# Kernel tuning notes

Measured on AMD Instinct MI355X. Metric: run time of the kernel, lower is better.

## Reference

```python
import jax, jax.numpy as jnp
import numpy as np

B, S, D, H = 8, 1024, 768, 12
DH = D // H  # 64
PATCHES = S  # module's `patches` arg; rows >= patches//2 are zeroed pre-softmax


def setup_inputs() -> dict:
    key = jax.random.key(0)
    ks = jax.random.split(key, 5)
    sc = 1.0 / np.sqrt(D)
    return {
        "hidden_states": jax.random.normal(ks[0], (B, S, D), dtype=jnp.float32),
        "Wq": jax.random.normal(ks[1], (D, D), dtype=jnp.float32) * sc,
        "bq": jnp.zeros((D,), dtype=jnp.float32),
        "Wk": jax.random.normal(ks[2], (D, D), dtype=jnp.float32) * sc,
        "bk": jnp.zeros((D,), dtype=jnp.float32),
        "Wv": jax.random.normal(ks[3], (D, D), dtype=jnp.float32) * sc,
        "bv": jnp.zeros((D,), dtype=jnp.float32),
        "Wo": jax.random.normal(ks[4], (D, D), dtype=jnp.float32) * sc,
        "bo": jnp.zeros((D,), dtype=jnp.float32),
    }


def _split_heads(x):
    # [B,S,D] -> [B,H,S,DH]
    b, s, _ = x.shape
    return x.reshape(b, s, H, DH).transpose(0, 2, 1, 3)


def reference(hidden_states, Wq, bq, Wk, bk, Wv, bv, Wo, bo):
    # self-attention path (kv=None), mask=None path, eval-mode dropout (identity)
    q = _split_heads(hidden_states @ Wq + bq)
    k = _split_heads(hidden_states @ Wk + bk)
    v = _split_heads(hidden_states @ Wv + bv)
    scores = jnp.einsum("bhqd,bhkd->bhqk", q, k) / np.sqrt(DH)
    # custom masking: zero out all score rows for query positions >= patches//2
    scores = scores.at[:, :, PATCHES // 2 :, :].set(0.0)
    probs = jax.nn.softmax(scores, axis=-1)
    ctx = jnp.einsum("bhqk,bhkd->bhqd", probs, v)
    ctx = ctx.transpose(0, 2, 1, 3).reshape(hidden_states.shape[0], -1, D)
    return ctx @ Wo + bo  # vis=False -> weights not returned
```

## Files before the change

kernel.cpp:

```cpp
#include <hip/hip_runtime.h>
#include <hip/hip_bf16.h>
#include <cstdint>


typedef __bf16 bf16_t;
typedef bf16_t bf16x8 __attribute__((ext_vector_type(8)));
typedef float f32x4 __attribute__((ext_vector_type(4)));

#define QSCALE 0.18033688011112042f

__device__ __forceinline__ f32x4 mfma16(bf16x8 a, bf16x8 b, f32x4 c) {
  return __builtin_amdgcn_mfma_f32_16x16x32_bf16(a, b, c, 0, 0, 0);
}
__device__ __forceinline__ unsigned packbf(float x, float y) {
  union { bf16_t h; unsigned short u; } a, b;
  a.h = (bf16_t)x; b.h = (bf16_t)y;
  return (unsigned)a.u | ((unsigned)b.u << 16);
}
__device__ __forceinline__ unsigned short tobf(float x) {
  union { bf16_t h; unsigned short u; } a; a.h = (bf16_t)x; return a.u;
}
__device__ __forceinline__ void glds16(const void* g, void* s) {
  __builtin_amdgcn_global_load_lds((const __attribute__((address_space(1))) void*)g,
                                   (__attribute__((address_space(3))) void*)s, 16, 0, 0);
}

__global__ __launch_bounds__(256) void k_cvt_x(const float* __restrict__ X,
                                               unsigned short* __restrict__ Xbf) {
  int i = blockIdx.x * 256 + threadIdx.x;
  const float4* p = (const float4*)X;
  float4 a = p[2 * i], b = p[2 * i + 1];
  uint4 o;
  o.x = packbf(a.x, a.y); o.y = packbf(a.z, a.w);
  o.z = packbf(b.x, b.y); o.w = packbf(b.z, b.w);
  ((uint4*)Xbf)[i] = o;
}

__global__ __launch_bounds__(256) void k_wtrans(const float* __restrict__ Wq,
                                                const float* __restrict__ Wk,
                                                const float* __restrict__ Wv,
                                                const float* __restrict__ Wo,
                                                unsigned short* __restrict__ Wt) {
  int which = blockIdx.z;
  const float* W = (which == 0) ? Wq : (which == 1) ? Wk : (which == 2) ? Wv : Wo;
  __shared__ float tile[64][65];
  int k0 = blockIdx.x * 64, n0 = blockIdx.y * 64;
  int t = threadIdx.x;
  int c = t & 63, r0 = t >> 6;
#pragma unroll
  for (int i = 0; i < 16; ++i) {
    int r = r0 + i * 4;
    tile[r][c] = W[(size_t)(k0 + r) * 768 + n0 + c];
  }
  __syncthreads();
#pragma unroll
  for (int i = 0; i < 16; ++i) {
    int nr = r0 + i * 4;
    Wt[(size_t)(which * 768 + n0 + nr) * 768 + k0 + c] = tobf(tile[c][nr]);
  }
}

__global__ __launch_bounds__(256) void k_gemm_qkv(
    const unsigned short* __restrict__ Xbf, const unsigned short* __restrict__ Wt,
    const float* __restrict__ bq, const float* __restrict__ bk, const float* __restrict__ bv,
    unsigned short* __restrict__ Qw, unsigned short* __restrict__ Kw,
    unsigned short* __restrict__ Vt) {
  __shared__ __align__(16) unsigned short As[4096], Bs[4096];
  int id = blockIdx.x;
  int mt, nt;
  if (id < 576) { int mf = id / 18; mt = ((mf >> 2) << 3) + (mf & 3); nt = id - mf * 18; }
  else { int j = id - 576; int mh = j / 12; mt = ((mh >> 2) << 3) + 4 + (mh & 3); nt = 6 + (j - mh * 12); }
  const int m0 = mt * 128, n0 = nt * 128;
  const int tid = threadIdx.x, w = tid >> 6, l = tid & 63, lr = l & 15, lg = l >> 4;
  const int wm = w >> 1, wn = w & 1;
  const unsigned short* gA = Xbf + (size_t)(m0 + (tid >> 2)) * 768 + (tid & 3) * 8;
  const unsigned short* gB = Wt + (size_t)(n0 + (tid >> 2)) * 768 + (tid & 3) * 8;
  unsigned short* sA = As + w * 512;
  unsigned short* sB = Bs + w * 512;
  const unsigned short* rA = As + (wm * 64 + lr) * 32 + lg * 8;
  const unsigned short* rB = Bs + (wn * 64 + lr) * 32 + lg * 8;
  f32x4 acc[4][4] = {};
  for (int kt = 0; kt < 24; ++kt) {
    const int ko = kt * 32;
    glds16(gA + ko, sA);            glds16(gA + 64 * 768 + ko, sA + 2048);
    glds16(gB + ko, sB);            glds16(gB + 64 * 768 + ko, sB + 2048);
    __syncthreads();
    bf16x8 af[4], bfr[4];
#pragma unroll
    for (int i = 0; i < 4; ++i) af[i] = *(const bf16x8*)(rA + i * 512);
#pragma unroll
    for (int i = 0; i < 4; ++i) bfr[i] = *(const bf16x8*)(rB + i * 512);
#pragma unroll
    for (int i = 0; i < 4; ++i)
#pragma unroll
      for (int j = 0; j < 4; ++j) acc[i][j] = mfma16(af[i], bfr[j], acc[i][j]);
    __syncthreads();
  }
  const int rbase = m0 + wm * 64 + lg * 4;
  const int cbase = n0 + wn * 64 + lr;
#pragma unroll
  for (int nf = 0; nf < 4; ++nf) {
    const int n = cbase + nf * 16;
#pragma unroll
    for (int mf = 0; mf < 4; ++mf) {
      const int r = rbase + mf * 16;
      const int b = r >> 10, s = r & 1023;
      if (n < 768) {
        const int h = n >> 6, dh = n & 63;
        const float bias = bq[n];
        unsigned short* qp = Qw + ((size_t)(b * 12 + h) * 512 + s) * 64 + dh;
#pragma unroll
        for (int rg = 0; rg < 4; ++rg)
          qp[(size_t)rg * 64] = tobf((acc[mf][nf][rg] + bias) * QSCALE);
      } else if (n < 1536) {
        const int d = n - 768, h = d >> 6, dh = d & 63;
        const float bias = bk[d];
        unsigned short* kp = Kw + ((size_t)(b * 12 + h) * 1024 + s) * 64 + dh;
#pragma unroll
        for (int rg = 0; rg < 4; ++rg)
          kp[(size_t)rg * 64] = tobf(acc[mf][nf][rg] + bias);
      } else {
        const int d = n - 1536, h = d >> 6, dh = d & 63;
        const float bias = bv[d];
        uint2 pv;
        pv.x = packbf(acc[mf][nf][0] + bias, acc[mf][nf][1] + bias);
        pv.y = packbf(acc[mf][nf][2] + bias, acc[mf][nf][3] + bias);
        *(uint2*)(Vt + ((size_t)(b * 12 + h) * 64 + dh) * 1024 + s) = pv;
      }
    }
  }
}

__global__ __launch_bounds__(256) void k_attn(const unsigned short* __restrict__ Qw,
                                              const unsigned short* __restrict__ Kw,
                                              const unsigned short* __restrict__ Vt,
                                              unsigned short* __restrict__ Ctx) {
  const int id = blockIdx.x;
  const int bh = id % 96;
  const int q0 = (id / 96) * 64;
  const int tid = threadIdx.x, w = tid >> 6, l = tid & 63, lr = l & 15, lg = l >> 4;
  const unsigned short* Qp = Qw + (size_t)bh * 512 * 64;
  const unsigned short* Kp = Kw + (size_t)bh * 1024 * 64;
  const unsigned short* Vp = Vt + (size_t)bh * 64 * 1024;

  __shared__ __align__(16) unsigned short Ks[2][4096];
  __shared__ __align__(16) unsigned short Vs[2][4096];
  __shared__ __align__(16) unsigned short P[4 * 16 * 72];

  const int j1 = 2 * w, j2 = 2 * w + 1;
  const int rA = j1 * 8 + (l >> 3), cA = (l & 7) ^ (rA & 7);
  const int rB = j2 * 8 + (l >> 3), cB = (l & 7) ^ (rB & 7);
  const unsigned short* kSrcA = Kp + rA * 64 + cA * 8;
  const unsigned short* kSrcB = Kp + rB * 64 + cB * 8;
  const unsigned short* vSrcA = Vp + rA * 1024 + cA * 8;
  const unsigned short* vSrcB = Vp + rB * 1024 + cB * 8;

  const int s0 = lr * 64 + ((lg ^ (lr & 7)) * 8);
  const int s1 = lr * 64 + (((lg + 4) ^ (lr & 7)) * 8);

  unsigned short* prow = P + (w * 16 + lr) * 72;
  const unsigned short* prd = prow + lg * 8;
  const int qrow = q0 + w * 16 + lr;
  const bf16x8 qf0 = *(const bf16x8*)(Qp + (size_t)qrow * 64 + lg * 8);
  const bf16x8 qf1 = *(const bf16x8*)(Qp + (size_t)qrow * 64 + 32 + lg * 8);

  f32x4 accc[4] = {};
  float z = 0.f;

  glds16(kSrcA, &Ks[0][j1 * 512]);
  glds16(kSrcB, &Ks[0][j2 * 512]);
  glds16(vSrcA, &Vs[0][j1 * 512]);
  glds16(vSrcB, &Vs[0][j2 * 512]);
  __syncthreads();

  for (int t = 0; t < 16; ++t) {
    const int pcur = t & 1;
    if (t < 15) {
      const int kv0 = (t + 1) * 64;
      glds16(kSrcA + (size_t)kv0 * 64, &Ks[1 - pcur][j1 * 512]);
      glds16(kSrcB + (size_t)kv0 * 64, &Ks[1 - pcur][j2 * 512]);
      glds16(vSrcA + kv0, &Vs[1 - pcur][j1 * 512]);
      glds16(vSrcB + kv0, &Vs[1 - pcur][j2 * 512]);
    }
    const unsigned short* Kb = Ks[pcur];
    const unsigned short* Vb = Vs[pcur];
    f32x4 ss[4] = {};
#pragma unroll
    for (int m = 0; m < 4; ++m) {
      bf16x8 k0 = *(const bf16x8*)(Kb + m * 1024 + s0);
      bf16x8 k1 = *(const bf16x8*)(Kb + m * 1024 + s1);
      ss[m] = mfma16(k0, qf0, ss[m]);
      ss[m] = mfma16(k1, qf1, ss[m]);
    }
#pragma unroll
    for (int m = 0; m < 4; ++m) {
      float p0 = exp2f(ss[m][0]), p1 = exp2f(ss[m][1]);
      float p2 = exp2f(ss[m][2]), p3 = exp2f(ss[m][3]);
      z += (p0 + p1) + (p2 + p3);
      uint2 pw;
      pw.x = packbf(p0, p1); pw.y = packbf(p2, p3);
      *(uint2*)(prow + m * 16 + lg * 4) = pw;
    }
    bf16x8 pb0 = *(const bf16x8*)prd;
    bf16x8 pb1 = *(const bf16x8*)(prd + 32);
#pragma unroll
    for (int m = 0; m < 4; ++m) {
      bf16x8 v0 = *(const bf16x8*)(Vb + m * 1024 + s0);
      bf16x8 v1 = *(const bf16x8*)(Vb + m * 1024 + s1);
      accc[m] = mfma16(v0, pb0, accc[m]);
      accc[m] = mfma16(v1, pb1, accc[m]);
    }
    __syncthreads();
  }

  z += __shfl_xor(z, 16, 64);
  z += __shfl_xor(z, 32, 64);
  const float zinv = 1.0f / z;
  const int b = bh / 12, h = bh - b * 12;
  unsigned short* crow = Ctx + ((size_t)b * 512 + qrow) * 768 + h * 64 + lg * 4;
#pragma unroll
  for (int m = 0; m < 4; ++m) {
    uint2 pv;
    pv.x = packbf(accc[m][0] * zinv, accc[m][1] * zinv);
    pv.y = packbf(accc[m][2] * zinv, accc[m][3] * zinv);
    *(uint2*)(crow + m * 16) = pv;
  }
}

__global__ __launch_bounds__(256) void k_meanv(const unsigned short* __restrict__ Vt,
                                               float* __restrict__ mv) {
  const int bh = blockIdx.x, tid = threadIdx.x;
  const int dh = tid >> 2, part = tid & 3;
  const bf16x8* p = (const bf16x8*)(Vt + ((size_t)bh * 64 + dh) * 1024 + part * 256);
  float s = 0.f;
#pragma unroll 4
  for (int i = 0; i < 32; ++i) {
    bf16x8 v = p[i];
#pragma unroll
    for (int j = 0; j < 8; ++j) s += (float)v[j];
  }
  s += __shfl_xor(s, 1, 64);
  s += __shfl_xor(s, 2, 64);
  if (part == 0) {
    const int b = bh / 12, h = bh - b * 12;
    mv[b * 768 + h * 64 + dh] = s * (1.f / 1024.f);
  }
}

__global__ __launch_bounds__(256) void k_orow(const float* __restrict__ mv,
                                              const float* __restrict__ Wo,
                                              const float* __restrict__ bo,
                                              float* __restrict__ orow) {
  const int b = blockIdx.x, n0 = blockIdx.y * 128;
  const int tid = threadIdx.x;
  __shared__ float mvs[768];
  for (int i = tid; i < 768; i += 256) mvs[i] = mv[b * 768 + i];
  __syncthreads();
  const int col = n0 + (tid >> 1);
  const int half = tid & 1;
  float a = 0.f;
  const int kend = half * 384 + 384;
  for (int k = half * 384; k < kend; ++k)
    a += mvs[k] * Wo[(size_t)k * 768 + col];
  a += __shfl_xor(a, 1, 64);
  if (half == 0) orow[b * 768 + col] = a + bo[col];
}

__global__ __launch_bounds__(256) void k_bcast(const float* __restrict__ orow,
                                               float* __restrict__ out) {
  int i = blockIdx.x * 256 + threadIdx.x;
  const int b = i / 98304;
  const int rem = i - b * 98304;
  const int s = rem / 192, dq = rem - s * 192;
  float4 v = ((const float4*)(orow + b * 768))[dq];
  ((float4*)(out + ((size_t)(b * 1024 + 512 + s)) * 768))[dq] = v;
}

__global__ __launch_bounds__(256) void k_gemm_o(const unsigned short* __restrict__ Ctx,
                                                const unsigned short* __restrict__ WtO,
                                                const float* __restrict__ bo,
                                                float* __restrict__ out) {
  __shared__ __align__(16) unsigned short As[4096], Bs[4096];
  const int m0 = blockIdx.x * 128, n0 = blockIdx.y * 128;
  const int tid = threadIdx.x, w = tid >> 6, l = tid & 63, lr = l & 15, lg = l >> 4;
  const int wm = w >> 1, wn = w & 1;
  const unsigned short* gA = Ctx + (size_t)(m0 + (tid >> 2)) * 768 + (tid & 3) * 8;
  const unsigned short* gB = WtO + (size_t)(n0 + (tid >> 2)) * 768 + (tid & 3) * 8;
  unsigned short* sA = As + w * 512;
  unsigned short* sB = Bs + w * 512;
  const unsigned short* rA = As + (wm * 64 + lr) * 32 + lg * 8;
  const unsigned short* rB = Bs + (wn * 64 + lr) * 32 + lg * 8;
  f32x4 acc[4][4] = {};
  for (int kt = 0; kt < 24; ++kt) {
    const int ko = kt * 32;
    glds16(gA + ko, sA);            glds16(gA + 64 * 768 + ko, sA + 2048);
    glds16(gB + ko, sB);            glds16(gB + 64 * 768 + ko, sB + 2048);
    __syncthreads();
    bf16x8 af[4], bfr[4];
#pragma unroll
    for (int i = 0; i < 4; ++i) af[i] = *(const bf16x8*)(rA + i * 512);
#pragma unroll
    for (int i = 0; i < 4; ++i) bfr[i] = *(const bf16x8*)(rB + i * 512);
#pragma unroll
    for (int i = 0; i < 4; ++i)
#pragma unroll
      for (int j = 0; j < 4; ++j) acc[i][j] = mfma16(af[i], bfr[j], acc[i][j]);
    __syncthreads();
  }
  const int rbase = m0 + wm * 64 + lg * 4;
  const int cbase = n0 + wn * 64 + lr;
#pragma unroll
  for (int nf = 0; nf < 4; ++nf) {
    const int n = cbase + nf * 16;
    const float bias = bo[n];
#pragma unroll
    for (int mf = 0; mf < 4; ++mf) {
      const int r = rbase + mf * 16;
      const int b = r >> 9, s = r & 511;
      float* op = out + ((size_t)b * 1024 + s) * 768 + n;
#pragma unroll
      for (int rg = 0; rg < 4; ++rg) op[(size_t)rg * 768] = acc[mf][nf][rg] + bias;
    }
  }
}

extern "C" void kernel_launch(void* const* d_in, const int* in_sizes, int n_in,
                              void* d_out, int out_size, void* d_ws, size_t ws_size,
                              hipStream_t stream) {
  const float* X  = (const float*)d_in[0];
  const float* Wq = (const float*)d_in[1];
  const float* bq = (const float*)d_in[2];
  const float* Wk = (const float*)d_in[3];
  const float* bk = (const float*)d_in[4];
  const float* Wv = (const float*)d_in[5];
  const float* bv = (const float*)d_in[6];
  const float* Wo = (const float*)d_in[7];
  const float* bo = (const float*)d_in[8];
  float* out = (float*)d_out;
  char* ws = (char*)d_ws;

  unsigned short* Xbf = (unsigned short*)(ws);
  unsigned short* Wt  = (unsigned short*)(ws + 12582912);
  unsigned short* Qw  = (unsigned short*)(ws + 17301504);
  unsigned short* Kw  = (unsigned short*)(ws + 23592960);
  unsigned short* Vt  = (unsigned short*)(ws + 36175872);
  unsigned short* Ctx = (unsigned short*)(ws + 48758784);
  float* mv   = (float*)(ws + 55050240);
  float* orow = (float*)(ws + 55074816);

  k_cvt_x<<<3072, 256, 0, stream>>>(X, Xbf);
  k_wtrans<<<dim3(12, 12, 4), 256, 0, stream>>>(Wq, Wk, Wv, Wo, Wt);
  k_gemm_qkv<<<960, 256, 0, stream>>>(Xbf, Wt, bq, bk, bv, Qw, Kw, Vt);
  k_attn<<<768, 256, 0, stream>>>(Qw, Kw, Vt, Ctx);
  k_meanv<<<96, 256, 0, stream>>>(Vt, mv);
  k_orow<<<dim3(8, 6), 256, 0, stream>>>(mv, Wo, bo, orow);
  k_bcast<<<3072, 256, 0, stream>>>(orow, out);
  k_gemm_o<<<dim3(32, 6), 256, 0, stream>>>(Ctx, Wt + (size_t)2304 * 768, bo, out);
}
```

Measured before the change: 227.3 us.

## Fuse prep kernels, fold V-mean into attention, merge tail broadcast, double QKV k-tile

Several changes land together. The X conversion and weight-transpose kernels are merged into one launch, the mean-of-V reduction is computed inside the first 96 attention blocks instead of a separate kernel, and the orow GEMV is fused with the broadcast that writes the masked output rows. The QKV GEMM now loads 64-wide K tiles per barrier, which halves the number of loop iterations and syncs at the cost of more LDS. The intent is to cut launch count and barrier overhead. The risks are that the broadcast now runs on only 48 blocks, and that the added V summation lengthens the first attention blocks.

```diff
diff --git a/kernel.cpp b/kernel.cpp
--- a/kernel.cpp
+++ b/kernel.cpp
@@ -25,26 +25,29 @@
                                    (__attribute__((address_space(3))) void*)s, 16, 0, 0);
 }
 
-__global__ __launch_bounds__(256) void k_cvt_x(const float* __restrict__ X,
-                                               unsigned short* __restrict__ Xbf) {
-  int i = blockIdx.x * 256 + threadIdx.x;
-  const float4* p = (const float4*)X;
-  float4 a = p[2 * i], b = p[2 * i + 1];
-  uint4 o;
-  o.x = packbf(a.x, a.y); o.y = packbf(a.z, a.w);
-  o.z = packbf(b.x, b.y); o.w = packbf(b.z, b.w);
-  ((uint4*)Xbf)[i] = o;
-}
-
-__global__ __launch_bounds__(256) void k_wtrans(const float* __restrict__ Wq,
-                                                const float* __restrict__ Wk,
-                                                const float* __restrict__ Wv,
-                                                const float* __restrict__ Wo,
-                                                unsigned short* __restrict__ Wt) {
-  int which = blockIdx.z;
+__global__ __launch_bounds__(256) void k_prep(const float* __restrict__ X,
+                                              const float* __restrict__ Wq,
+                                              const float* __restrict__ Wk,
+                                              const float* __restrict__ Wv,
+                                              const float* __restrict__ Wo,
+                                              unsigned short* __restrict__ Xbf,
+                                              unsigned short* __restrict__ Wt) {
+  __shared__ float tile[64][65];
+  if (blockIdx.x < 3072) {
+    int i = blockIdx.x * 256 + threadIdx.x;
+    const float4* p = (const float4*)X;
+    float4 a = p[2 * i], b = p[2 * i + 1];
+    uint4 o;
+    o.x = packbf(a.x, a.y); o.y = packbf(a.z, a.w);
+    o.z = packbf(b.x, b.y); o.w = packbf(b.z, b.w);
+    ((uint4*)Xbf)[i] = o;
+    return;
+  }
+  int id = blockIdx.x - 3072;
+  int which = id / 144;
+  int rem = id - which * 144;
   const float* W = (which == 0) ? Wq : (which == 1) ? Wk : (which == 2) ? Wv : Wo;
-  __shared__ float tile[64][65];
-  int k0 = blockIdx.x * 64, n0 = blockIdx.y * 64;
+  int k0 = (rem / 12) * 64, n0 = (rem % 12) * 64;
   int t = threadIdx.x;
   int c = t & 63, r0 = t >> 6;
 #pragma unroll
@@ -65,7 +68,7 @@
     const float* __restrict__ bq, const float* __restrict__ bk, const float* __restrict__ bv,
     unsigned short* __restrict__ Qw, unsigned short* __restrict__ Kw,
     unsigned short* __restrict__ Vt) {
-  __shared__ __align__(16) unsigned short As[4096], Bs[4096];
+  __shared__ __align__(16) unsigned short As[8192], Bs[8192];
   int id = blockIdx.x;
   int mt, nt;
   if (id < 576) { int mf = id / 18; mt = ((mf >> 2) << 3) + (mf & 3); nt = id - mf * 18; }
@@ -73,27 +76,33 @@
   const int m0 = mt * 128, n0 = nt * 128;
   const int tid = threadIdx.x, w = tid >> 6, l = tid & 63, lr = l & 15, lg = l >> 4;
   const int wm = w >> 1, wn = w & 1;
-  const unsigned short* gA = Xbf + (size_t)(m0 + (tid >> 2)) * 768 + (tid & 3) * 8;
-  const unsigned short* gB = Wt + (size_t)(n0 + (tid >> 2)) * 768 + (tid & 3) * 8;
-  unsigned short* sA = As + w * 512;
-  unsigned short* sB = Bs + w * 512;
+  const unsigned short* gA = Xbf + (size_t)(m0 + (l >> 2)) * 768 + (l & 3) * 8;
+  const unsigned short* gB = Wt + (size_t)(n0 + (l >> 2)) * 768 + (l & 3) * 8;
+  const size_t rlo = (size_t)(w * 16) * 768, rhi = (size_t)((4 + w) * 16) * 768;
+  unsigned short* sA0 = As + w * 512;
+  unsigned short* sB0 = Bs + w * 512;
   const unsigned short* rA = As + (wm * 64 + lr) * 32 + lg * 8;
   const unsigned short* rB = Bs + (wn * 64 + lr) * 32 + lg * 8;
   f32x4 acc[4][4] = {};
-  for (int kt = 0; kt < 24; ++kt) {
-    const int ko = kt * 32;
-    glds16(gA + ko, sA);            glds16(gA + 64 * 768 + ko, sA + 2048);
-    glds16(gB + ko, sB);            glds16(gB + 64 * 768 + ko, sB + 2048);
-    __syncthreads();
-    bf16x8 af[4], bfr[4];
-#pragma unroll
-    for (int i = 0; i < 4; ++i) af[i] = *(const bf16x8*)(rA + i * 512);
-#pragma unroll
-    for (int i = 0; i < 4; ++i) bfr[i] = *(const bf16x8*)(rB + i * 512);
-#pragma unroll
-    for (int i = 0; i < 4; ++i)
-#pragma unroll
-      for (int j = 0; j < 4; ++j) acc[i][j] = mfma16(af[i], bfr[j], acc[i][j]);
+  for (int kt = 0; kt < 12; ++kt) {
+    const int ko = kt * 64;
+    glds16(gA + rlo + ko, sA0);            glds16(gA + rhi + ko, sA0 + 2048);
+    glds16(gA + rlo + ko + 32, sA0 + 4096); glds16(gA + rhi + ko + 32, sA0 + 6144);
+    glds16(gB + rlo + ko, sB0);            glds16(gB + rhi + ko, sB0 + 2048);
+    glds16(gB + rlo + ko + 32, sB0 + 4096); glds16(gB + rhi + ko + 32, sB0 + 6144);
+    __syncthreads();
+#pragma unroll
+    for (int kh = 0; kh < 2; ++kh) {
+      bf16x8 af[4], bfr[4];
+#pragma unroll
+      for (int i = 0; i < 4; ++i) af[i] = *(const bf16x8*)(rA + kh * 4096 + i * 512);
+#pragma unroll
+      for (int i = 0; i < 4; ++i) bfr[i] = *(const bf16x8*)(rB + kh * 4096 + i * 512);
+#pragma unroll
+      for (int i = 0; i < 4; ++i)
+#pragma unroll
+        for (int j = 0; j < 4; ++j) acc[i][j] = mfma16(af[i], bfr[j], acc[i][j]);
+    }
     __syncthreads();
   }
   const int rbase = m0 + wm * 64 + lg * 4;
@@ -134,7 +143,8 @@
 __global__ __launch_bounds__(256) void k_attn(const unsigned short* __restrict__ Qw,
                                               const unsigned short* __restrict__ Kw,
                                               const unsigned short* __restrict__ Vt,
-                                              unsigned short* __restrict__ Ctx) {
+                                              unsigned short* __restrict__ Ctx,
+                                              float* __restrict__ mv) {
   const int id = blockIdx.x;
   const int bh = id % 96;
   const int q0 = (id / 96) * 64;
@@ -165,6 +175,7 @@
   const bf16x8 qf1 = *(const bf16x8*)(Qp + (size_t)qrow * 64 + 32 + lg * 8);
 
   f32x4 accc[4] = {};
+  float vs0 = 0.f, vs1 = 0.f, vs2 = 0.f, vs3 = 0.f;
   float z = 0.f;
 
   glds16(kSrcA, &Ks[0][j1 * 512]);
@@ -207,16 +218,37 @@
     for (int m = 0; m < 4; ++m) {
       bf16x8 v0 = *(const bf16x8*)(Vb + m * 1024 + s0);
       bf16x8 v1 = *(const bf16x8*)(Vb + m * 1024 + s1);
+      if (id < 96) {
+        float sv = 0.f;
+#pragma unroll
+        for (int jj = 0; jj < 8; ++jj) sv += (float)v0[jj] + (float)v1[jj];
+        if (m == 0) vs0 += sv; else if (m == 1) vs1 += sv;
+        else if (m == 2) vs2 += sv; else vs3 += sv;
+      }
       accc[m] = mfma16(v0, pb0, accc[m]);
       accc[m] = mfma16(v1, pb1, accc[m]);
     }
     __syncthreads();
+  }
+
+  const int b = bh / 12, h = bh - b * 12;
+  if (id < 96) {
+    vs0 += __shfl_xor(vs0, 16, 64); vs0 += __shfl_xor(vs0, 32, 64);
+    vs1 += __shfl_xor(vs1, 16, 64); vs1 += __shfl_xor(vs1, 32, 64);
+    vs2 += __shfl_xor(vs2, 16, 64); vs2 += __shfl_xor(vs2, 32, 64);
+    vs3 += __shfl_xor(vs3, 16, 64); vs3 += __shfl_xor(vs3, 32, 64);
+    if (w == 0 && lg == 0) {
+      float* mp = mv + b * 768 + h * 64 + lr;
+      mp[0] = vs0 * (1.f / 1024.f);
+      mp[16] = vs1 * (1.f / 1024.f);
+      mp[32] = vs2 * (1.f / 1024.f);
+      mp[48] = vs3 * (1.f / 1024.f);
+    }
   }
 
   z += __shfl_xor(z, 16, 64);
   z += __shfl_xor(z, 32, 64);
   const float zinv = 1.0f / z;
-  const int b = bh / 12, h = bh - b * 12;
   unsigned short* crow = Ctx + ((size_t)b * 512 + qrow) * 768 + h * 64 + lg * 4;
 #pragma unroll
   for (int m = 0; m < 4; ++m) {
@@ -227,33 +259,14 @@
   }
 }
 
-__global__ __launch_bounds__(256) void k_meanv(const unsigned short* __restrict__ Vt,
-                                               float* __restrict__ mv) {
-  const int bh = blockIdx.x, tid = threadIdx.x;
-  const int dh = tid >> 2, part = tid & 3;
-  const bf16x8* p = (const bf16x8*)(Vt + ((size_t)bh * 64 + dh) * 1024 + part * 256);
-  float s = 0.f;
-#pragma unroll 4
-  for (int i = 0; i < 32; ++i) {
-    bf16x8 v = p[i];
-#pragma unroll
-    for (int j = 0; j < 8; ++j) s += (float)v[j];
-  }
-  s += __shfl_xor(s, 1, 64);
-  s += __shfl_xor(s, 2, 64);
-  if (part == 0) {
-    const int b = bh / 12, h = bh - b * 12;
-    mv[b * 768 + h * 64 + dh] = s * (1.f / 1024.f);
-  }
-}
-
-__global__ __launch_bounds__(256) void k_orow(const float* __restrict__ mv,
+__global__ __launch_bounds__(256) void k_tail(const float* __restrict__ mv,
                                               const float* __restrict__ Wo,
                                               const float* __restrict__ bo,
-                                              float* __restrict__ orow) {
+                                              float* __restrict__ out) {
   const int b = blockIdx.x, n0 = blockIdx.y * 128;
   const int tid = threadIdx.x;
   __shared__ float mvs[768];
+  __shared__ float cvals[128];
   for (int i = tid; i < 768; i += 256) mvs[i] = mv[b * 768 + i];
   __syncthreads();
   const int col = n0 + (tid >> 1);
@@ -263,17 +276,13 @@
   for (int k = half * 384; k < kend; ++k)
     a += mvs[k] * Wo[(size_t)k * 768 + col];
   a += __shfl_xor(a, 1, 64);
-  if (half == 0) orow[b * 768 + col] = a + bo[col];
-}
-
-__global__ __launch_bounds__(256) void k_bcast(const float* __restrict__ orow,
-                                               float* __restrict__ out) {
-  int i = blockIdx.x * 256 + threadIdx.x;
-  const int b = i / 98304;
-  const int rem = i - b * 98304;
-  const int s = rem / 192, dq = rem - s * 192;
-  float4 v = ((const float4*)(orow + b * 768))[dq];
-  ((float4*)(out + ((size_t)(b * 1024 + 512 + s)) * 768))[dq] = v;
+  if (half == 0) cvals[col - n0] = a + bo[col];
+  __syncthreads();
+  const float4 c4 = ((const float4*)cvals)[tid & 31];
+  const int srow = tid >> 5;
+  float* obase = out + ((size_t)b * 1024 + 512 + srow) * 768 + n0;
+  for (int r = 0; r < 512; r += 8)
+    ((float4*)(obase + (size_t)r * 768))[tid & 31] = c4;
 }
 
 __global__ __launch_bounds__(256) void k_gemm_o(const unsigned short* __restrict__ Ctx,
@@ -346,14 +355,10 @@
   unsigned short* Vt  = (unsigned short*)(ws + 36175872);
   unsigned short* Ctx = (unsigned short*)(ws + 48758784);
   float* mv   = (float*)(ws + 55050240);
-  float* orow = (float*)(ws + 55074816);
-
-  k_cvt_x<<<3072, 256, 0, stream>>>(X, Xbf);
-  k_wtrans<<<dim3(12, 12, 4), 256, 0, stream>>>(Wq, Wk, Wv, Wo, Wt);
+
+  k_prep<<<3648, 256, 0, stream>>>(X, Wq, Wk, Wv, Wo, Xbf, Wt);
   k_gemm_qkv<<<960, 256, 0, stream>>>(Xbf, Wt, bq, bk, bv, Qw, Kw, Vt);
-  k_attn<<<768, 256, 0, stream>>>(Qw, Kw, Vt, Ctx);
-  k_meanv<<<96, 256, 0, stream>>>(Vt, mv);
-  k_orow<<<dim3(8, 6), 256, 0, stream>>>(mv, Wo, bo, orow);
-  k_bcast<<<3072, 256, 0, stream>>>(orow, out);
+  k_attn<<<768, 256, 0, stream>>>(Qw, Kw, Vt, Ctx, mv);
+  k_tail<<<dim3(8, 6), 256, 0, stream>>>(mv, Wo, bo, out);
   k_gemm_o<<<dim3(32, 6), 256, 0, stream>>>(Ctx, Wt + (size_t)2304 * 768, bo, out);
 }
```

Result: faster. 213.8 us (-6.0%).
